# Kernel tuning notes

Measured on AMD Instinct MI355X. Metric: run time of the kernel, lower is better.

## Reference

```python
import jax, jax.numpy as jnp
import numpy as np
import math

A = 256            # n_agents == batch rows (epymarl stacks agents along batch)
B = A
OBS = 512          # obs_shape = (input_shape - n_actions) // 2
NA = 64            # n_actions
MSG = 2048         # messages_shape (divisible by A)
H = 1024           # hidden_dim
T = 3              # trajectory_length
TAU = OBS + NA
VD = MSG // A      # per-agent message dim


def setup_inputs() -> dict:
    key = jax.random.key(0)
    keys = iter(jax.random.split(key, 40))
    def lin(o, i):
        w = jax.random.normal(next(keys), (o, i), jnp.float32) * (i ** -0.5)
        return w, jnp.zeros((o,), jnp.float32)
    d = {}
    d["inputs"] = jax.random.normal(next(keys), (B, 2 * OBS + NA + MSG), jnp.float32)
    d["hidden_state"] = jax.random.normal(next(keys), (B, 3 * H), jnp.float32) * 0.1
    for name, o, i in [("pi_fc1", H, OBS + MSG), ("pi_fc2", NA, H),
                       ("fa_fc1", H, OBS), ("fa_fc2", (A - 1) * NA, H),
                       ("fo_fc1", H, NA * A + OBS), ("fo_fc2", OBS, H),
                       ("am_qs", H, MSG), ("am_ks", H, TAU), ("am_vs", VD, TAU)]:
        d[name + "_w"], d[name + "_b"] = lin(o, i)
    for name in ["pi_rnn", "fa_rnn", "fo_rnn"]:
        d[name + "_wih"], d[name + "_bih"] = lin(3 * H, H)
        d[name + "_whh"], d[name + "_bhh"] = lin(3 * H, H)
    return d


def _gru(x, h, wih, whh, bih, bhh):
    gi = x @ wih.T + bih
    gh = h @ whh.T + bhh
    ir, iz, i_n = jnp.split(gi, 3, -1)
    hr, hz, h_n = jnp.split(gh, 3, -1)
    r = jax.nn.sigmoid(ir + hr)
    z = jax.nn.sigmoid(iz + hz)
    n = jnp.tanh(i_n + r * h_n)
    return (1.0 - z) * n + z * h


def reference(inputs, hidden_state,
              pi_fc1_w, pi_fc1_b, pi_fc2_w, pi_fc2_b,
              pi_rnn_wih, pi_rnn_whh, pi_rnn_bih, pi_rnn_bhh,
              fa_fc1_w, fa_fc1_b, fa_fc2_w, fa_fc2_b,
              fa_rnn_wih, fa_rnn_whh, fa_rnn_bih, fa_rnn_bhh,
              fo_fc1_w, fo_fc1_b, fo_fc2_w, fo_fc2_b,
              fo_rnn_wih, fo_rnn_whh, fo_rnn_bih, fo_rnn_bhh,
              am_qs_w, am_qs_b, am_ks_w, am_ks_b, am_vs_w, am_vs_b):
    sg = jax.lax.stop_gradient
    lin = lambda x, w, b: x @ w.T + b
    h_fa = hidden_state[:, :H]
    h_fo = hidden_state[:, H:2 * H]
    h_pi0 = hidden_state[:, -H:]
    obs = inputs[:, :OBS]
    prev_obs = inputs[:, OBS:2 * OBS]
    prev_act = sg(inputs[:, 2 * OBS:2 * OBS + NA])   # .detach() in torch
    prev_msg = inputs[:, -MSG:]

    def pi(o, m, h):
        x = jax.nn.relu(lin(jnp.concatenate([o, m], -1), pi_fc1_w, pi_fc1_b))
        h2 = _gru(x, h, pi_rnn_wih, pi_rnn_whh, pi_rnn_bih, pi_rnn_bhh)
        return lin(h2, pi_fc2_w, pi_fc2_b), h2

    # ---- ImaginedTrajectory rollout (fixed small T, python loop is structural) ----
    o, a, h_pi = prev_obs, prev_act, h_pi0
    observations, actions = [o], [a]
    for _ in range(T - 1):
        x = jax.nn.relu(lin(o, fa_fc1_w, fa_fc1_b))
        h_fa = _gru(x, h_fa, fa_rnn_wih, fa_rnn_whh, fa_rnn_bih, fa_rnn_bhh)
        q = lin(h_fa, fa_fc2_w, fa_fc2_b)                       # [B,(A-1)*NA]
        qs = jax.nn.softmax(q.reshape(B, A - 1, NA), -1)
        # torch stack(qs_out).reshape(orig): scrambles (A-1,B) order, kept faithfully
        fa = jnp.transpose(qs, (1, 0, 2)).reshape(B, (A - 1) * NA)
        x2 = jax.nn.relu(lin(jnp.concatenate([fa, a, o], -1), fo_fc1_w, fo_fc1_b))
        h_fo = _gru(x2, h_fo, fo_rnn_wih, fo_rnn_whh, fo_rnn_bih, fo_rnn_bhh)
        nxt_o = lin(h_fo, fo_fc2_w, fo_fc2_b)
        nxt_a, h_pi = pi(sg(o), sg(prev_msg), sg(h_pi))         # forward_pi detaches inputs
        o, a = nxt_o, nxt_a
        observations.append(o)
        actions.append(a)
    taus = jnp.stack([jnp.concatenate([observations[t], actions[t]], -1)
                      for t in range(T)])                        # [T,B,TAU]

    # ---- AttentionMechanism: batched equivalent of the per-agent python loops ----
    # k rows are indexed j*n_agents + i with batch == n_agents, i.e. k[t, b] here.
    qv = lin(prev_msg, am_qs_w, am_qs_b)                         # [B,H]
    kk = jnp.einsum('tbi,hi->tbh', taus, am_ks_w) + am_ks_b      # [T,B,H]
    vv = jnp.einsum('tbi,vi->tbv', taus, am_vs_w) + am_vs_b      # [T,B,VD]
    alpha = jax.nn.softmax(jnp.einsum('bh,tbh->bt', qv, kk) / math.sqrt(H), -1)
    new_message = jnp.einsum('bt,tbv->bv', alpha, vv)            # [B,VD]

    # cat([msg]*A, 0).reshape(B,-1): each agent receives all agents' messages
    pi_msg = jnp.tile(new_message, (A, 1)).reshape(B, -1)        # [B,MSG]
    action, h_pi_f = pi(obs, pi_msg, h_pi0)                      # uses ORIGINAL h_pi slice
    h_out = jnp.concatenate([h_fa, h_fo, h_pi_f], -1)            # [B,3H]
    q_out = jnp.concatenate([new_message, action], -1)           # [B,VD+NA]
    return q_out, h_out
```

## Files before the change

kernel.cpp:

```cpp
#include <hip/hip_runtime.h>
#include <hip/hip_bf16.h>
#include <math.h>

#define OBS 512
#define MSG 2048
#define TAU 576
#define TAUP 640
#define QN 16320
#define X2W 16896
#define INW 3136
#define PIW 2560

typedef short short8v __attribute__((ext_vector_type(8)));
typedef float f32x4 __attribute__((ext_vector_type(4)));

__device__ inline unsigned bfbits(float x) {
  __hip_bfloat16 h = __float2bfloat16(x);
  return (unsigned)*reinterpret_cast<unsigned short*>(&h);
}

__device__ inline void gload16(const void* g, void* l) {
  __builtin_amdgcn_global_load_lds((__attribute__((address_space(1))) void*)(g),
                                   (__attribute__((address_space(3))) void*)(l), 16, 0, 0);
}

template<int ACT, bool ATOMIC>
__global__ __launch_bounds__(256)
void k_mfma(const __hip_bfloat16* __restrict__ A, int lda,
            const __hip_bfloat16* __restrict__ Wt, int ldw,
            const float* __restrict__ bias,
            float* __restrict__ C, int ldc,
            __hip_bfloat16* __restrict__ Cb, int ldcb,
            int Nlim, int nsteps)
{
  __shared__ __hip_bfloat16 As[2][64 * 128];
  __shared__ __hip_bfloat16 Bs[2][64 * 128];
  const int tid = threadIdx.x;
  const int lane = tid & 63;
  const int wid = tid >> 6;
  const int m0 = blockIdx.y * 64, n0 = blockIdx.x * 64;
  const int wr = wid >> 1, wc = wid & 1;
  const int fr = lane & 15, q = lane >> 4;
  const size_t k0 = (size_t)blockIdx.z * nsteps * 128;

  const __hip_bfloat16* Ab = A + (size_t)m0 * lda + k0;
  const __hip_bfloat16* Bb = Wt + (size_t)n0 * ldw + k0;

  int srow[4], scol[4], sdst[4];
#pragma unroll
  for (int r = 0; r < 4; ++r) {
    int chunk = r * 256 + tid;
    srow[r] = chunk >> 4;
    int c = chunk & 15;
    scol[r] = (c ^ (srow[r] & 7)) * 8;
    sdst[r] = chunk * 8;
  }

  const int arow0 = wr * 32 + fr, arow1 = arow0 + 16;
  const int brow0 = wc * 32 + fr, brow1 = brow0 + 16;
  const int amask = arow0 & 7, bmask = brow0 & 7;

  f32x4 acc[2][2] = {};

#pragma unroll
  for (int r = 0; r < 4; ++r)
    gload16(Ab + (size_t)srow[r] * lda + scol[r], &As[0][sdst[r]]);
#pragma unroll
  for (int r = 0; r < 4; ++r)
    gload16(Bb + (size_t)srow[r] * ldw + scol[r], &Bs[0][sdst[r]]);
  __syncthreads();

  for (int t = 0; t < nsteps; ++t) {
    if (t + 1 < nsteps) {
      const int kt = (t + 1) * 128;
      const int buf = (t + 1) & 1;
#pragma unroll
      for (int r = 0; r < 4; ++r)
        gload16(Ab + (size_t)srow[r] * lda + kt + scol[r], &As[buf][sdst[r]]);
#pragma unroll
      for (int r = 0; r < 4; ++r)
        gload16(Bb + (size_t)srow[r] * ldw + kt + scol[r], &Bs[buf][sdst[r]]);
    }
    const __hip_bfloat16* Ac = As[t & 1];
    const __hip_bfloat16* Bc = Bs[t & 1];
#pragma unroll
    for (int ks = 0; ks < 4; ++ks) {
      const int cc = ks * 4 + q;
      short8v a0 = *(const short8v*)&Ac[arow0 * 128 + ((cc ^ amask) << 3)];
      short8v a1 = *(const short8v*)&Ac[arow1 * 128 + ((cc ^ amask) << 3)];
      short8v b0 = *(const short8v*)&Bc[brow0 * 128 + ((cc ^ bmask) << 3)];
      short8v b1 = *(const short8v*)&Bc[brow1 * 128 + ((cc ^ bmask) << 3)];
      acc[0][0] = __builtin_amdgcn_mfma_f32_16x16x32_bf16(a0, b0, acc[0][0], 0, 0, 0);
      acc[0][1] = __builtin_amdgcn_mfma_f32_16x16x32_bf16(a0, b1, acc[0][1], 0, 0, 0);
      acc[1][0] = __builtin_amdgcn_mfma_f32_16x16x32_bf16(a1, b0, acc[1][0], 0, 0, 0);
      acc[1][1] = __builtin_amdgcn_mfma_f32_16x16x32_bf16(a1, b1, acc[1][1], 0, 0, 0);
    }
    __syncthreads();
  }

#pragma unroll
  for (int i = 0; i < 2; ++i) {
    const int mbase = m0 + wr * 32 + i * 16 + q * 4;
#pragma unroll
    for (int j = 0; j < 2; ++j) {
      const int n = n0 + wc * 32 + j * 16 + fr;
      if (n >= Nlim) continue;
      if (ATOMIC) {
#pragma unroll
        for (int v = 0; v < 4; ++v)
          atomicAdd(&C[(size_t)(mbase + v) * ldc + n], acc[i][j][v]);
      } else {
        const float bb = bias[n];
#pragma unroll
        for (int v = 0; v < 4; ++v) {
          float val = acc[i][j][v] + bb;
          if (ACT) val = fmaxf(val, 0.f);
          if (C)  C[(size_t)(mbase + v) * ldc + n] = val;
          if (Cb) Cb[(size_t)(mbase + v) * ldcb + n] = __float2bfloat16(val);
        }
      }
    }
  }
}

__global__ __launch_bounds__(256)
void k_cvtw(const float* __restrict__ src, int lds_, __hip_bfloat16* __restrict__ dst,
            int N, int Kdst, int Kval, int Npad)
{
  size_t idx = ((size_t)blockIdx.x * 256 + threadIdx.x) * 8;
  if (idx >= (size_t)Npad * Kdst) return;
  int n = (int)(idx / Kdst);
  int k = (int)(idx % Kdst);
  uint4 o;
  if (n < N && k < Kval) {
    const float* s = src + (size_t)n * lds_ + k;
    float4 v0 = *(const float4*)s;
    float4 v1 = *(const float4*)(s + 4);
    o.x = bfbits(v0.x) | (bfbits(v0.y) << 16);
    o.y = bfbits(v0.z) | (bfbits(v0.w) << 16);
    o.z = bfbits(v1.x) | (bfbits(v1.y) << 16);
    o.w = bfbits(v1.z) | (bfbits(v1.w) << 16);
  } else {
    o = make_uint4(0, 0, 0, 0);
  }
  *(uint4*)(dst + idx) = o;
}

__global__ __launch_bounds__(256)
void k_gru(const float* __restrict__ gi, const float* __restrict__ gh,
           const float* __restrict__ hs, int ldsrc,
           float* __restrict__ hd, int lddst, __hip_bfloat16* __restrict__ hb)
{
  int idx = blockIdx.x * 256 + threadIdx.x;
  int b = idx >> 10, j = idx & 1023;
  float ir = gi[b * 3072 + j];
  float iz = gi[b * 3072 + 1024 + j];
  float in_ = gi[b * 3072 + 2048 + j];
  float hr = gh[b * 3072 + j];
  float hz = gh[b * 3072 + 1024 + j];
  float hn = gh[b * 3072 + 2048 + j];
  float r = 1.f / (1.f + expf(-(ir + hr)));
  float z = 1.f / (1.f + expf(-(iz + hz)));
  float n = tanhf(in_ + r * hn);
  float h = hs[(size_t)b * ldsrc + j];
  float o = (1.f - z) * n + z * h;
  hd[(size_t)b * lddst + j] = o;
  hb[idx] = __float2bfloat16(o);
}

__global__ __launch_bounds__(256)
void k_softmax_scatter(const __hip_bfloat16* __restrict__ q, __hip_bfloat16* __restrict__ x2)
{
  int wid = blockIdx.x * 4 + (threadIdx.x >> 6);
  int lane = threadIdx.x & 63;
  int b = wid / 255, p = wid % 255;
  float v = __bfloat162float(q[(size_t)b * QN + p * 64 + lane]);
  float m = v;
#pragma unroll
  for (int s = 32; s; s >>= 1) m = fmaxf(m, __shfl_xor(m, s));
  float e = expf(v - m);
  float sum = e;
#pragma unroll
  for (int s = 32; s; s >>= 1) sum += __shfl_xor(sum, s);
  float r = e / sum;
  int flat = p * 16384 + b * 64 + lane;
  int bp = flat / QN;
  int j = flat - bp * QN;
  x2[(size_t)bp * X2W + j] = __float2bfloat16(r);
}

__global__ __launch_bounds__(256)
void k_x2_tail(const __hip_bfloat16* __restrict__ taus_t, __hip_bfloat16* __restrict__ x2)
{
  int idx = blockIdx.x * 256 + threadIdx.x;
  int b = idx / TAU, c = idx % TAU;
  if (c < 64)
    x2[(size_t)b * X2W + QN + c] = taus_t[(size_t)b * TAUP + OBS + c];
  else
    x2[(size_t)b * X2W + QN + 64 + (c - 64)] = taus_t[(size_t)b * TAUP + (c - 64)];
}

__global__ __launch_bounds__(256)
void k_concat_pi_loop(const __hip_bfloat16* __restrict__ taus_t,
                      const __hip_bfloat16* __restrict__ msg,
                      __hip_bfloat16* __restrict__ piin)
{
  int idx = blockIdx.x * 256 + threadIdx.x;
  int b = idx / PIW, c = idx % PIW;
  piin[idx] = (c < OBS) ? taus_t[(size_t)b * TAUP + c] : msg[b * MSG + (c - OBS)];
}

__global__ __launch_bounds__(256)
void k_concat_pi_final(const float* __restrict__ in, const float* __restrict__ nm,
                       __hip_bfloat16* __restrict__ piin)
{
  int idx = blockIdx.x * 256 + threadIdx.x;
  int b = idx / PIW, c = idx % PIW;
  float v = (c < OBS) ? in[(size_t)b * INW + c] : nm[c - OBS];
  piin[idx] = __float2bfloat16(v);
}

__global__ __launch_bounds__(256)
void k_init_h(const float* __restrict__ hid,
              float* __restrict__ h32a, float* __restrict__ h32o, float* __restrict__ h32p,
              __hip_bfloat16* __restrict__ hba, __hip_bfloat16* __restrict__ hbo,
              __hip_bfloat16* __restrict__ hbp, __hip_bfloat16* __restrict__ hbp0)
{
  int idx = blockIdx.x * 256 + threadIdx.x;
  int b = idx / 3072, c = idx % 3072;
  float v = hid[idx];
  __hip_bfloat16 hb = __float2bfloat16(v);
  int j = c & 1023;
  if (c < 1024)      { h32a[b * 1024 + j] = v; hba[b * 1024 + j] = hb; }
  else if (c < 2048) { h32o[b * 1024 + j] = v; hbo[b * 1024 + j] = hb; }
  else               { h32p[b * 1024 + j] = v; hbp[b * 1024 + j] = hb; hbp0[b * 1024 + j] = hb; }
}

__global__ __launch_bounds__(256)
void k_init_taus(const float* __restrict__ in, __hip_bfloat16* __restrict__ taus)
{
  int idx = blockIdx.x * 256 + threadIdx.x;
  int t = idx / (256 * TAUP);
  int r = (idx / TAUP) % 256;
  int c = idx % TAUP;
  float v = 0.f;
  if (t == 0 && c < TAU)
    v = (c < OBS) ? in[(size_t)r * INW + OBS + c]
                  : in[(size_t)r * INW + 2 * OBS + (c - OBS)];
  taus[idx] = __float2bfloat16(v);
}

__global__ __launch_bounds__(256)
void k_fill_bias(float* __restrict__ C, const float* __restrict__ bias)
{
  int idx = blockIdx.x * 256 + threadIdx.x;
  C[idx] = bias[idx & 1023];
}

__global__ __launch_bounds__(256)
void k_relu_cvt(const float* __restrict__ s, __hip_bfloat16* __restrict__ d)
{
  int idx = blockIdx.x * 256 + threadIdx.x;
  d[idx] = __float2bfloat16(fmaxf(s[idx], 0.f));
}

__global__ __launch_bounds__(64)
void k_vv(const __hip_bfloat16* __restrict__ taus, const float* __restrict__ w,
          const float* __restrict__ bias, float* __restrict__ vv)
{
  int row = blockIdx.x;
  int lane = threadIdx.x;
  const __hip_bfloat16* tr = taus + (size_t)row * TAUP;
  for (int v = 0; v < 8; ++v) {
    float s = 0.f;
    for (int k = lane; k < TAU; k += 64) s += __bfloat162float(tr[k]) * w[v * TAU + k];
#pragma unroll
    for (int d = 32; d; d >>= 1) s += __shfl_xor(s, d);
    if (lane == 0) vv[row * 8 + v] = s + bias[v];
  }
}

__global__ __launch_bounds__(64)
void k_attn(const float* __restrict__ qv, const float* __restrict__ kk,
            const float* __restrict__ vv, float* __restrict__ nm,
            float* __restrict__ out_q)
{
  int b = blockIdx.x;
  int lane = threadIdx.x;
  const float* qb = qv + (size_t)b * 1024;
  float s[3];
#pragma unroll
  for (int t = 0; t < 3; ++t) {
    const float* kb = kk + (size_t)(t * 256 + b) * 1024;
    float acc = 0.f;
    for (int h = lane; h < 1024; h += 64) acc += qb[h] * kb[h];
#pragma unroll
    for (int d = 32; d; d >>= 1) acc += __shfl_xor(acc, d);
    s[t] = acc * (1.f / 32.f);
  }
  float m = fmaxf(s[0], fmaxf(s[1], s[2]));
  float e0 = expf(s[0] - m), e1 = expf(s[1] - m), e2 = expf(s[2] - m);
  float inv = 1.f / (e0 + e1 + e2);
  float a0 = e0 * inv, a1 = e1 * inv, a2 = e2 * inv;
  if (lane < 8) {
    float v = a0 * vv[(0 * 256 + b) * 8 + lane]
            + a1 * vv[(1 * 256 + b) * 8 + lane]
            + a2 * vv[(2 * 256 + b) * 8 + lane];
    nm[b * 8 + lane] = v;
    out_q[b * 72 + lane] = v;
  }
}

__global__ __launch_bounds__(256)
void k_copy_hout(const float* __restrict__ hfa, const float* __restrict__ hfo,
                 float* __restrict__ hout)
{
  int idx = blockIdx.x * 256 + threadIdx.x;
  int b = idx / 2048, c = idx % 2048;
  float v = (c < 1024) ? hfa[b * 1024 + c] : hfo[b * 1024 + (c - 1024)];
  hout[(size_t)b * 3072 + c] = v;
}

extern "C" void kernel_launch(void* const* d_in, const int* in_sizes, int n_in,
                              void* d_out_v, int out_size, void* d_ws, size_t ws_size,
                              hipStream_t stream)
{
  const float* inputs   = (const float*)d_in[0];
  const float* hidden   = (const float*)d_in[1];
  const float* pi_fc1_w = (const float*)d_in[2];
  const float* pi_fc1_b = (const float*)d_in[3];
  const float* pi_fc2_w = (const float*)d_in[4];
  const float* pi_fc2_b = (const float*)d_in[5];
  const float* fa_fc1_w = (const float*)d_in[6];
  const float* fa_fc1_b = (const float*)d_in[7];
  const float* fa_fc2_w = (const float*)d_in[8];
  const float* fa_fc2_b = (const float*)d_in[9];
  const float* fo_fc1_w = (const float*)d_in[10];
  const float* fo_fc1_b = (const float*)d_in[11];
  const float* fo_fc2_w = (const float*)d_in[12];
  const float* fo_fc2_b = (const float*)d_in[13];
  const float* am_qs_w  = (const float*)d_in[14];
  const float* am_qs_b  = (const float*)d_in[15];
  const float* am_ks_w  = (const float*)d_in[16];
  const float* am_ks_b  = (const float*)d_in[17];
  const float* am_vs_w  = (const float*)d_in[18];
  const float* am_vs_b  = (const float*)d_in[19];
  const float* pi_wih   = (const float*)d_in[20];
  const float* pi_bih   = (const float*)d_in[21];
  const float* pi_whh   = (const float*)d_in[22];
  const float* pi_bhh   = (const float*)d_in[23];
  const float* fa_wih   = (const float*)d_in[24];
  const float* fa_bih   = (const float*)d_in[25];
  const float* fa_whh   = (const float*)d_in[26];
  const float* fa_bhh   = (const float*)d_in[27];
  const float* fo_wih   = (const float*)d_in[28];
  const float* fo_bih   = (const float*)d_in[29];
  const float* fo_whh   = (const float*)d_in[30];
  const float* fo_bhh   = (const float*)d_in[31];

  float* out = (float*)d_out_v;
  char* p = (char*)d_ws;
  auto alloc = [&](size_t bytes) { void* r = p; p += (bytes + 255) & ~(size_t)255; return r; };
  typedef __hip_bfloat16 bf;

  bf* WPI1 = (bf*)alloc((size_t)1024 * 2560 * 2);
  bf* WPI2 = (bf*)alloc((size_t)64 * 1024 * 2);
  bf* WFA1 = (bf*)alloc((size_t)1024 * 512 * 2);
  bf* WFA2 = (bf*)alloc((size_t)16320 * 1024 * 2);
  bf* WFO1 = (bf*)alloc((size_t)1024 * 16896 * 2);
  bf* WFO2 = (bf*)alloc((size_t)512 * 1024 * 2);
  bf* WQS  = (bf*)alloc((size_t)1024 * 2048 * 2);
  bf* WKS  = (bf*)alloc((size_t)1024 * TAUP * 2);
  bf* WPIIH = (bf*)alloc((size_t)3072 * 1024 * 2);
  bf* WPIHH = (bf*)alloc((size_t)3072 * 1024 * 2);
  bf* WFAIH = (bf*)alloc((size_t)3072 * 1024 * 2);
  bf* WFAHH = (bf*)alloc((size_t)3072 * 1024 * 2);
  bf* WFOIH = (bf*)alloc((size_t)3072 * 1024 * 2);
  bf* WFOHH = (bf*)alloc((size_t)3072 * 1024 * 2);
  bf* HFAB = (bf*)alloc((size_t)256 * 1024 * 2);
  bf* HFOB = (bf*)alloc((size_t)256 * 1024 * 2);
  bf* HPIB = (bf*)alloc((size_t)256 * 1024 * 2);
  bf* HPI0B = (bf*)alloc((size_t)256 * 1024 * 2);
  bf* XBUFB = (bf*)alloc((size_t)256 * 1024 * 2);
  bf* TAUSB = (bf*)alloc((size_t)3 * 256 * TAUP * 2);
  bf* X2B  = (bf*)alloc((size_t)256 * X2W * 2);
  bf* PIINB = (bf*)alloc((size_t)256 * PIW * 2);
  bf* MSGB = (bf*)alloc((size_t)256 * MSG * 2);
  bf* QBUFB = (bf*)alloc((size_t)256 * QN * 2);
  float* HFA32 = (float*)alloc((size_t)256 * 1024 * 4);
  float* HFO32 = (float*)alloc((size_t)256 * 1024 * 4);
  float* HPI32 = (float*)alloc((size_t)256 * 1024 * 4);
  float* XBUF32 = (float*)alloc((size_t)256 * 1024 * 4);
  float* GI = (float*)alloc((size_t)256 * 3072 * 4);
  float* GH = (float*)alloc((size_t)256 * 3072 * 4);
  float* QV = (float*)alloc((size_t)256 * 1024 * 4);
  float* KK = (float*)alloc((size_t)768 * 1024 * 4);
  float* VV = (float*)alloc((size_t)768 * 8 * 4);
  float* NM = (float*)alloc((size_t)2048 * 4);

  auto cvt = [&](const float* src, int srcld, bf* dst, int N, int Kdst, int Kval, int Npad) {
    size_t total = ((size_t)Npad * Kdst) / 8;
    int blocks = (int)((total + 255) / 256);
    k_cvtw<<<blocks, 256, 0, stream>>>(src, srcld, dst, N, Kdst, Kval, Npad);
  };
  auto mm = [&](const bf* Aa, int lda, const bf* Ww, int ldw, const float* bias,
                float* C, int ldc, bf* Cb, int ldcb,
                int M, int Npad, int Nlim, int K, int act) {
    dim3 g(Npad / 64, M / 64, 1);
    int nsteps = K / 128;
    if (act) k_mfma<1, false><<<g, 256, 0, stream>>>(Aa, lda, Ww, ldw, bias, C, ldc, Cb, ldcb, Nlim, nsteps);
    else     k_mfma<0, false><<<g, 256, 0, stream>>>(Aa, lda, Ww, ldw, bias, C, ldc, Cb, ldcb, Nlim, nsteps);
  };

  cvt(pi_fc1_w, 2560, WPI1, 1024, 2560, 2560, 1024);
  cvt(pi_fc2_w, 1024, WPI2, 64, 1024, 1024, 64);
  cvt(fa_fc1_w, 512,  WFA1, 1024, 512, 512, 1024);
  cvt(fa_fc2_w, 1024, WFA2, 16320, 1024, 1024, 16320);
  cvt(fo_fc1_w, 16896, WFO1, 1024, 16896, 16896, 1024);
  cvt(fo_fc2_w, 1024, WFO2, 512, 1024, 1024, 512);
  cvt(am_qs_w, 2048, WQS, 1024, 2048, 2048, 1024);
  cvt(am_ks_w, 576, WKS, 1024, TAUP, 576, 1024);
  cvt(pi_wih, 1024, WPIIH, 3072, 1024, 1024, 3072);
  cvt(pi_whh, 1024, WPIHH, 3072, 1024, 1024, 3072);
  cvt(fa_wih, 1024, WFAIH, 3072, 1024, 1024, 3072);
  cvt(fa_whh, 1024, WFAHH, 3072, 1024, 1024, 3072);
  cvt(fo_wih, 1024, WFOIH, 3072, 1024, 1024, 3072);
  cvt(fo_whh, 1024, WFOHH, 3072, 1024, 1024, 3072);
  cvt(inputs + 1088, INW, MSGB, 256, 2048, 2048, 256);

  k_init_h<<<3072, 256, 0, stream>>>(hidden, HFA32, HFO32, HPI32, HFAB, HFOB, HPIB, HPI0B);
  k_init_taus<<<3 * TAUP, 256, 0, stream>>>(inputs, TAUSB);

  for (int t = 0; t < 2; ++t) {
    bf* taus_t = TAUSB + (size_t)t * 256 * TAUP;
    bf* taus_n = TAUSB + (size_t)(t + 1) * 256 * TAUP;
    mm(taus_t, TAUP, WFA1, 512, fa_fc1_b, nullptr, 0, XBUFB, 1024, 256, 1024, 1024, 512, 1);
    mm(XBUFB, 1024, WFAIH, 1024, fa_bih, GI, 3072, nullptr, 0, 256, 3072, 3072, 1024, 0);
    mm(HFAB, 1024, WFAHH, 1024, fa_bhh, GH, 3072, nullptr, 0, 256, 3072, 3072, 1024, 0);
    k_gru<<<1024, 256, 0, stream>>>(GI, GH, HFA32, 1024, HFA32, 1024, HFAB);
    mm(HFAB, 1024, WFA2, 1024, fa_fc2_b, nullptr, 0, QBUFB, QN, 256, QN, QN, 1024, 0);
    k_x2_tail<<<576, 256, 0, stream>>>(taus_t, X2B);
    k_softmax_scatter<<<16320, 256, 0, stream>>>(QBUFB, X2B);
    k_fill_bias<<<1024, 256, 0, stream>>>(XBUF32, fo_fc1_b);
    {
      dim3 g(1024 / 64, 256 / 64, 12);
      k_mfma<0, true><<<g, 256, 0, stream>>>(X2B, X2W, WFO1, X2W, nullptr,
                                             XBUF32, 1024, nullptr, 0, 1024, 11);
    }
    k_relu_cvt<<<1024, 256, 0, stream>>>(XBUF32, XBUFB);
    mm(XBUFB, 1024, WFOIH, 1024, fo_bih, GI, 3072, nullptr, 0, 256, 3072, 3072, 1024, 0);
    mm(HFOB, 1024, WFOHH, 1024, fo_bhh, GH, 3072, nullptr, 0, 256, 3072, 3072, 1024, 0);
    k_gru<<<1024, 256, 0, stream>>>(GI, GH, HFO32, 1024, HFO32, 1024, HFOB);
    mm(HFOB, 1024, WFO2, 1024, fo_fc2_b, nullptr, 0, taus_n, TAUP, 256, 512, 512, 1024, 0);
    k_concat_pi_loop<<<2560, 256, 0, stream>>>(taus_t, MSGB, PIINB);
    mm(PIINB, PIW, WPI1, PIW, pi_fc1_b, nullptr, 0, XBUFB, 1024, 256, 1024, 1024, 2560, 1);
    mm(XBUFB, 1024, WPIIH, 1024, pi_bih, GI, 3072, nullptr, 0, 256, 3072, 3072, 1024, 0);
    mm(HPIB, 1024, WPIHH, 1024, pi_bhh, GH, 3072, nullptr, 0, 256, 3072, 3072, 1024, 0);
    k_gru<<<1024, 256, 0, stream>>>(GI, GH, HPI32, 1024, HPI32, 1024, HPIB);
    mm(HPIB, 1024, WPI2, 1024, pi_fc2_b, nullptr, 0, taus_n + OBS, TAUP, 256, 64, 64, 1024, 0);
  }

  mm(MSGB, MSG, WQS, MSG, am_qs_b, QV, 1024, nullptr, 0, 256, 1024, 1024, 2048, 0);
  mm(TAUSB, TAUP, WKS, TAUP, am_ks_b, KK, 1024, nullptr, 0, 768, 1024, 1024, TAUP, 0);
  k_vv<<<768, 64, 0, stream>>>(TAUSB, am_vs_w, am_vs_b, VV);
  k_attn<<<256, 64, 0, stream>>>(QV, KK, VV, NM, out);

  k_concat_pi_final<<<2560, 256, 0, stream>>>(inputs, NM, PIINB);
  mm(PIINB, PIW, WPI1, PIW, pi_fc1_b, nullptr, 0, XBUFB, 1024, 256, 1024, 1024, 2560, 1);
  mm(XBUFB, 1024, WPIIH, 1024, pi_bih, GI, 3072, nullptr, 0, 256, 3072, 3072, 1024, 0);
  mm(HPI0B, 1024, WPIHH, 1024, pi_bhh, GH, 3072, nullptr, 0, 256, 3072, 3072, 1024, 0);
  k_gru<<<1024, 256, 0, stream>>>(GI, GH, hidden + 2048, 3072,
                                  out + 256 * 72 + 2048, 3072, HPIB);
  mm(HPIB, 1024, WPI2, 1024, pi_fc2_b, out + 8, 72, nullptr, 0, 256, 64, 64, 1024, 0);
  k_copy_hout<<<2048, 256, 0, stream>>>(HFA32, HFO32, out + 256 * 72);
  (void)in_sizes; (void)n_in; (void)out_size; (void)ws_size;
}
```

Before: 626.2 us.

## Retile GEMM to 256x64 blocks, fuse GRU gate GEMMs, batch weight conversion

```diff
diff --git a/kernel.cpp b/kernel.cpp
--- a/kernel.cpp
+++ b/kernel.cpp
@@ -24,83 +24,89 @@
                                    (__attribute__((address_space(3))) void*)(l), 16, 0, 0);
 }
 
-template<int ACT, bool ATOMIC>
-__global__ __launch_bounds__(256)
-void k_mfma(const __hip_bfloat16* __restrict__ A, int lda,
-            const __hip_bfloat16* __restrict__ Wt, int ldw,
-            const float* __restrict__ bias,
-            float* __restrict__ C, int ldc,
-            __hip_bfloat16* __restrict__ Cb, int ldcb,
-            int Nlim, int nsteps)
-{
-  __shared__ __hip_bfloat16 As[2][64 * 128];
-  __shared__ __hip_bfloat16 Bs[2][64 * 128];
+struct MMSet {
+  const __hip_bfloat16* A;
+  const __hip_bfloat16* W;
+  const float* bias;
+  float* C;
+  __hip_bfloat16* Cb;
+  int lda, ldw, ldc, ldcb;
+};
+
+template<int ACT, bool ATOMIC, bool DUAL>
+__global__ __launch_bounds__(512)
+void k_mm(MMSet s0, MMSet s1, int Nlim, int kSteps)
+{
+  __shared__ __hip_bfloat16 As[2][256 * 64];
+  __shared__ __hip_bfloat16 Bs[2][64 * 64];
+  const MMSet S = (DUAL && blockIdx.z) ? s1 : s0;
   const int tid = threadIdx.x;
   const int lane = tid & 63;
   const int wid = tid >> 6;
-  const int m0 = blockIdx.y * 64, n0 = blockIdx.x * 64;
+  const int m0 = blockIdx.y * 256;
+  const int n0 = blockIdx.x * 64;
+  const size_t k0 = ATOMIC ? (size_t)blockIdx.z * kSteps * 64 : 0;
+
+  const __hip_bfloat16* Ab = S.A + (size_t)m0 * S.lda + k0;
+  const __hip_bfloat16* Bb = S.W + (size_t)n0 * S.ldw + k0;
+
+  int arow[4], acol[4], adst[4];
+#pragma unroll
+  for (int r = 0; r < 4; ++r) {
+    int chunk = r * 512 + tid;
+    arow[r] = chunk >> 3;
+    acol[r] = ((chunk & 7) ^ (arow[r] & 7)) * 8;
+    adst[r] = chunk * 8;
+  }
+  const int brow = tid >> 3;
+  const int bcol = ((tid & 7) ^ (brow & 7)) * 8;
+  const int bdst = tid * 8;
+
   const int wr = wid >> 1, wc = wid & 1;
   const int fr = lane & 15, q = lane >> 4;
-  const size_t k0 = (size_t)blockIdx.z * nsteps * 128;
-
-  const __hip_bfloat16* Ab = A + (size_t)m0 * lda + k0;
-  const __hip_bfloat16* Bb = Wt + (size_t)n0 * ldw + k0;
-
-  int srow[4], scol[4], sdst[4];
-#pragma unroll
-  for (int r = 0; r < 4; ++r) {
-    int chunk = r * 256 + tid;
-    srow[r] = chunk >> 4;
-    int c = chunk & 15;
-    scol[r] = (c ^ (srow[r] & 7)) * 8;
-    sdst[r] = chunk * 8;
-  }
-
-  const int arow0 = wr * 32 + fr, arow1 = arow0 + 16;
-  const int brow0 = wc * 32 + fr, brow1 = brow0 + 16;
-  const int amask = arow0 & 7, bmask = brow0 & 7;
-
-  f32x4 acc[2][2] = {};
-
-#pragma unroll
-  for (int r = 0; r < 4; ++r)
-    gload16(Ab + (size_t)srow[r] * lda + scol[r], &As[0][sdst[r]]);
-#pragma unroll
-  for (int r = 0; r < 4; ++r)
-    gload16(Bb + (size_t)srow[r] * ldw + scol[r], &Bs[0][sdst[r]]);
+  const int xm = fr & 7;
+
+  f32x4 acc[4][2] = {};
+
+  auto stage = [&](int buf, int kt) {
+#pragma unroll
+    for (int r = 0; r < 4; ++r)
+      gload16(Ab + (size_t)arow[r] * S.lda + kt + acol[r], &As[buf][adst[r]]);
+    gload16(Bb + (size_t)brow * S.ldw + kt + bcol, &Bs[buf][bdst]);
+  };
+
+  stage(0, 0);
   __syncthreads();
 
-  for (int t = 0; t < nsteps; ++t) {
-    if (t + 1 < nsteps) {
-      const int kt = (t + 1) * 128;
-      const int buf = (t + 1) & 1;
-#pragma unroll
-      for (int r = 0; r < 4; ++r)
-        gload16(Ab + (size_t)srow[r] * lda + kt + scol[r], &As[buf][sdst[r]]);
-#pragma unroll
-      for (int r = 0; r < 4; ++r)
-        gload16(Bb + (size_t)srow[r] * ldw + kt + scol[r], &Bs[buf][sdst[r]]);
-    }
+  for (int t = 0; t < kSteps; ++t) {
+    if (t + 1 < kSteps) stage((t + 1) & 1, (t + 1) * 64);
     const __hip_bfloat16* Ac = As[t & 1];
     const __hip_bfloat16* Bc = Bs[t & 1];
 #pragma unroll
-    for (int ks = 0; ks < 4; ++ks) {
+    for (int ks = 0; ks < 2; ++ks) {
       const int cc = ks * 4 + q;
-      short8v a0 = *(const short8v*)&Ac[arow0 * 128 + ((cc ^ amask) << 3)];
-      short8v a1 = *(const short8v*)&Ac[arow1 * 128 + ((cc ^ amask) << 3)];
-      short8v b0 = *(const short8v*)&Bc[brow0 * 128 + ((cc ^ bmask) << 3)];
-      short8v b1 = *(const short8v*)&Bc[brow1 * 128 + ((cc ^ bmask) << 3)];
+      const int co = ((cc ^ xm) << 3);
+      short8v a0 = *(const short8v*)&Ac[(wr * 64 +  0 + fr) * 64 + co];
+      short8v a1 = *(const short8v*)&Ac[(wr * 64 + 16 + fr) * 64 + co];
+      short8v a2 = *(const short8v*)&Ac[(wr * 64 + 32 + fr) * 64 + co];
+      short8v a3 = *(const short8v*)&Ac[(wr * 64 + 48 + fr) * 64 + co];
+      short8v b0 = *(const short8v*)&Bc[(wc * 32 +  0 + fr) * 64 + co];
+      short8v b1 = *(const short8v*)&Bc[(wc * 32 + 16 + fr) * 64 + co];
       acc[0][0] = __builtin_amdgcn_mfma_f32_16x16x32_bf16(a0, b0, acc[0][0], 0, 0, 0);
       acc[0][1] = __builtin_amdgcn_mfma_f32_16x16x32_bf16(a0, b1, acc[0][1], 0, 0, 0);
       acc[1][0] = __builtin_amdgcn_mfma_f32_16x16x32_bf16(a1, b0, acc[1][0], 0, 0, 0);
       acc[1][1] = __builtin_amdgcn_mfma_f32_16x16x32_bf16(a1, b1, acc[1][1], 0, 0, 0);
+      acc[2][0] = __builtin_amdgcn_mfma_f32_16x16x32_bf16(a2, b0, acc[2][0], 0, 0, 0);
+      acc[2][1] = __builtin_amdgcn_mfma_f32_16x16x32_bf16(a2, b1, acc[2][1], 0, 0, 0);
+      acc[3][0] = __builtin_amdgcn_mfma_f32_16x16x32_bf16(a3, b0, acc[3][0], 0, 0, 0);
+      acc[3][1] = __builtin_amdgcn_mfma_f32_16x16x32_bf16(a3, b1, acc[3][1], 0, 0, 0);
     }
     __syncthreads();
   }
 
 #pragma unroll
-  for (int i = 0; i < 2; ++i) {
-    const int mbase = m0 + wr * 32 + i * 16 + q * 4;
+  for (int i = 0; i < 4; ++i) {
+    const int mb = m0 + wr * 64 + i * 16 + q * 4;
 #pragma unroll
     for (int j = 0; j < 2; ++j) {
       const int n = n0 + wc * 32 + j * 16 + fr;
@@ -108,32 +114,51 @@
       if (ATOMIC) {
 #pragma unroll
         for (int v = 0; v < 4; ++v)
-          atomicAdd(&C[(size_t)(mbase + v) * ldc + n], acc[i][j][v]);
+          atomicAdd(&S.C[(size_t)(mb + v) * S.ldc + n], acc[i][j][v]);
       } else {
-        const float bb = bias[n];
+        const float bb = S.bias[n];
 #pragma unroll
         for (int v = 0; v < 4; ++v) {
           float val = acc[i][j][v] + bb;
           if (ACT) val = fmaxf(val, 0.f);
-          if (C)  C[(size_t)(mbase + v) * ldc + n] = val;
-          if (Cb) Cb[(size_t)(mbase + v) * ldcb + n] = __float2bfloat16(val);
+          if (S.C)  S.C[(size_t)(mb + v) * S.ldc + n] = val;
+          if (S.Cb) S.Cb[(size_t)(mb + v) * S.ldcb + n] = __float2bfloat16(val);
         }
       }
     }
   }
 }
 
-__global__ __launch_bounds__(256)
-void k_cvtw(const float* __restrict__ src, int lds_, __hip_bfloat16* __restrict__ dst,
-            int N, int Kdst, int Kval, int Npad)
-{
-  size_t idx = ((size_t)blockIdx.x * 256 + threadIdx.x) * 8;
-  if (idx >= (size_t)Npad * Kdst) return;
-  int n = (int)(idx / Kdst);
-  int k = (int)(idx % Kdst);
+struct CvtTable {
+  const float* src[15];
+  __hip_bfloat16* dst[15];
+  long nchunk[15];
+  int srcld[15], N[15], Kdst[15], Kval[15];
+  int cumBlk[16];
+};
+
+__global__ __launch_bounds__(256)
+void k_cvt_all(CvtTable T)
+{
+  const int bx = blockIdx.x;
+  int sg = 0;
+#pragma unroll
+  for (int i = 1; i < 15; ++i) sg += (bx >= T.cumBlk[i]) ? 1 : 0;
+  const float* src = T.src[0]; __hip_bfloat16* dst = T.dst[0];
+  long nchunk = T.nchunk[0];
+  int srcld = T.srcld[0], N = T.N[0], Kd = T.Kdst[0], Kv = T.Kval[0], b0 = T.cumBlk[0];
+#pragma unroll
+  for (int i = 1; i < 15; ++i)
+    if (sg == i) { src = T.src[i]; dst = T.dst[i]; nchunk = T.nchunk[i];
+                   srcld = T.srcld[i]; N = T.N[i]; Kd = T.Kdst[i]; Kv = T.Kval[i]; b0 = T.cumBlk[i]; }
+  long chunk = (long)(bx - b0) * 256 + threadIdx.x;
+  if (chunk >= nchunk) return;
+  long idx = chunk * 8;
+  int n = (int)(idx / Kd);
+  int k = (int)(idx % Kd);
   uint4 o;
-  if (n < N && k < Kval) {
-    const float* s = src + (size_t)n * lds_ + k;
+  if (n < N && k < Kv) {
+    const float* s = src + (size_t)n * srcld + k;
     float4 v0 = *(const float4*)s;
     float4 v1 = *(const float4*)(s + 4);
     o.x = bfbits(v0.x) | (bfbits(v0.y) << 16);
@@ -366,7 +391,7 @@
   bf* WPI1 = (bf*)alloc((size_t)1024 * 2560 * 2);
   bf* WPI2 = (bf*)alloc((size_t)64 * 1024 * 2);
   bf* WFA1 = (bf*)alloc((size_t)1024 * 512 * 2);
-  bf* WFA2 = (bf*)alloc((size_t)16320 * 1024 * 2);
+  bf* WFA2 = (bf*)alloc((size_t)16384 * 1024 * 2);
   bf* WFO1 = (bf*)alloc((size_t)1024 * 16896 * 2);
   bf* WFO2 = (bf*)alloc((size_t)512 * 1024 * 2);
   bf* WQS  = (bf*)alloc((size_t)1024 * 2048 * 2);
@@ -398,80 +423,93 @@
   float* VV = (float*)alloc((size_t)768 * 8 * 4);
   float* NM = (float*)alloc((size_t)2048 * 4);
 
-  auto cvt = [&](const float* src, int srcld, bf* dst, int N, int Kdst, int Kval, int Npad) {
-    size_t total = ((size_t)Npad * Kdst) / 8;
-    int blocks = (int)((total + 255) / 256);
-    k_cvtw<<<blocks, 256, 0, stream>>>(src, srcld, dst, N, Kdst, Kval, Npad);
+  CvtTable T;
+  int nseg = 0; int blk = 0;
+  auto addseg = [&](const float* src, int srcld, bf* dst, int N, int Kdst, int Kval, int Npad) {
+    long ch = (long)Npad * Kdst / 8;
+    T.src[nseg] = src; T.dst[nseg] = dst; T.nchunk[nseg] = ch;
+    T.srcld[nseg] = srcld; T.N[nseg] = N; T.Kdst[nseg] = Kdst; T.Kval[nseg] = Kval;
+    T.cumBlk[nseg] = blk;
+    blk += (int)((ch + 255) / 256);
+    ++nseg;
   };
-  auto mm = [&](const bf* Aa, int lda, const bf* Ww, int ldw, const float* bias,
-                float* C, int ldc, bf* Cb, int ldcb,
-                int M, int Npad, int Nlim, int K, int act) {
-    dim3 g(Npad / 64, M / 64, 1);
-    int nsteps = K / 128;
-    if (act) k_mfma<1, false><<<g, 256, 0, stream>>>(Aa, lda, Ww, ldw, bias, C, ldc, Cb, ldcb, Nlim, nsteps);
-    else     k_mfma<0, false><<<g, 256, 0, stream>>>(Aa, lda, Ww, ldw, bias, C, ldc, Cb, ldcb, Nlim, nsteps);
+  addseg(pi_fc1_w, 2560, WPI1, 1024, 2560, 2560, 1024);
+  addseg(pi_fc2_w, 1024, WPI2, 64, 1024, 1024, 64);
+  addseg(fa_fc1_w, 512,  WFA1, 1024, 512, 512, 1024);
+  addseg(fa_fc2_w, 1024, WFA2, 16320, 1024, 1024, 16384);
+  addseg(fo_fc1_w, 16896, WFO1, 1024, 16896, 16896, 1024);
+  addseg(fo_fc2_w, 1024, WFO2, 512, 1024, 1024, 512);
+  addseg(am_qs_w, 2048, WQS, 1024, 2048, 2048, 1024);
+  addseg(am_ks_w, 576, WKS, 1024, TAUP, 576, 1024);
+  addseg(pi_wih, 1024, WPIIH, 3072, 1024, 1024, 3072);
+  addseg(pi_whh, 1024, WPIHH, 3072, 1024, 1024, 3072);
+  addseg(fa_wih, 1024, WFAIH, 3072, 1024, 1024, 3072);
+  addseg(fa_whh, 1024, WFAHH, 3072, 1024, 1024, 3072);
+  addseg(fo_wih, 1024, WFOIH, 3072, 1024, 1024, 3072);
+  addseg(fo_whh, 1024, WFOHH, 3072, 1024, 1024, 3072);
+  addseg(inputs + 1088, INW, MSGB, 256, 2048, 2048, 256);
+  T.cumBlk[15] = blk;
+
+  auto mset = [&](const bf* A, int lda, const bf* W, int ldw, const float* bias,
+                  float* C, int ldc, bf* Cb, int ldcb) {
+    MMSet s; s.A = A; s.W = W; s.bias = bias; s.C = C; s.Cb = Cb;
+    s.lda = lda; s.ldw = ldw; s.ldc = ldc; s.ldcb = ldcb; return s;
   };
-
-  cvt(pi_fc1_w, 2560, WPI1, 1024, 2560, 2560, 1024);
-  cvt(pi_fc2_w, 1024, WPI2, 64, 1024, 1024, 64);
-  cvt(fa_fc1_w, 512,  WFA1, 1024, 512, 512, 1024);
-  cvt(fa_fc2_w, 1024, WFA2, 16320, 1024, 1024, 16320);
-  cvt(fo_fc1_w, 16896, WFO1, 1024, 16896, 16896, 1024);
-  cvt(fo_fc2_w, 1024, WFO2, 512, 1024, 1024, 512);
-  cvt(am_qs_w, 2048, WQS, 1024, 2048, 2048, 1024);
-  cvt(am_ks_w, 576, WKS, 1024, TAUP, 576, 1024);
-  cvt(pi_wih, 1024, WPIIH, 3072, 1024, 1024, 3072);
-  cvt(pi_whh, 1024, WPIHH, 3072, 1024, 1024, 3072);
-  cvt(fa_wih, 1024, WFAIH, 3072, 1024, 1024, 3072);
-  cvt(fa_whh, 1024, WFAHH, 3072, 1024, 1024, 3072);
-  cvt(fo_wih, 1024, WFOIH, 3072, 1024, 1024, 3072);
-  cvt(fo_whh, 1024, WFOHH, 3072, 1024, 1024, 3072);
-  cvt(inputs + 1088, INW, MSGB, 256, 2048, 2048, 256);
-
+  auto mm = [&](MMSet a, int M, int Npad, int Nlim, int K, int act) {
+    dim3 g(Npad / 64, M / 256, 1);
+    if (act) k_mm<1, false, false><<<g, 512, 0, stream>>>(a, a, Nlim, K / 64);
+    else     k_mm<0, false, false><<<g, 512, 0, stream>>>(a, a, Nlim, K / 64);
+  };
+  auto mmDual = [&](MMSet a, MMSet b, int Npad, int K) {
+    dim3 g(Npad / 64, 1, 2);
+    k_mm<0, false, true><<<g, 512, 0, stream>>>(a, b, Npad, K / 64);
+  };
+
+  k_cvt_all<<<blk, 256, 0, stream>>>(T);
   k_init_h<<<3072, 256, 0, stream>>>(hidden, HFA32, HFO32, HPI32, HFAB, HFOB, HPIB, HPI0B);
   k_init_taus<<<3 * TAUP, 256, 0, stream>>>(inputs, TAUSB);
 
   for (int t = 0; t < 2; ++t) {
     bf* taus_t = TAUSB + (size_t)t * 256 * TAUP;
     bf* taus_n = TAUSB + (size_t)(t + 1) * 256 * TAUP;
-    mm(taus_t, TAUP, WFA1, 512, fa_fc1_b, nullptr, 0, XBUFB, 1024, 256, 1024, 1024, 512, 1);
-    mm(XBUFB, 1024, WFAIH, 1024, fa_bih, GI, 3072, nullptr, 0, 256, 3072, 3072, 1024, 0);
-    mm(HFAB, 1024, WFAHH, 1024, fa_bhh, GH, 3072, nullptr, 0, 256, 3072, 3072, 1024, 0);
+    mm(mset(taus_t, TAUP, WFA1, 512, fa_fc1_b, nullptr, 0, XBUFB, 1024), 256, 1024, 1024, 512, 1);
+    mmDual(mset(XBUFB, 1024, WFAIH, 1024, fa_bih, GI, 3072, nullptr, 0),
+           mset(HFAB, 1024, WFAHH, 1024, fa_bhh, GH, 3072, nullptr, 0), 3072, 1024);
     k_gru<<<1024, 256, 0, stream>>>(GI, GH, HFA32, 1024, HFA32, 1024, HFAB);
-    mm(HFAB, 1024, WFA2, 1024, fa_fc2_b, nullptr, 0, QBUFB, QN, 256, QN, QN, 1024, 0);
+    mm(mset(HFAB, 1024, WFA2, 1024, fa_fc2_b, nullptr, 0, QBUFB, QN), 256, 16384, QN, 1024, 0);
     k_x2_tail<<<576, 256, 0, stream>>>(taus_t, X2B);
     k_softmax_scatter<<<16320, 256, 0, stream>>>(QBUFB, X2B);
     k_fill_bias<<<1024, 256, 0, stream>>>(XBUF32, fo_fc1_b);
     {
-      dim3 g(1024 / 64, 256 / 64, 12);
-      k_mfma<0, true><<<g, 256, 0, stream>>>(X2B, X2W, WFO1, X2W, nullptr,
-                                             XBUF32, 1024, nullptr, 0, 1024, 11);
+      dim3 g(16, 1, 12);
+      MMSet s = mset(X2B, X2W, WFO1, X2W, fo_fc1_b, XBUF32, 1024, nullptr, 0);
+      k_mm<0, true, false><<<g, 512, 0, stream>>>(s, s, 1024, 22);
     }
     k_relu_cvt<<<1024, 256, 0, stream>>>(XBUF32, XBUFB);
-    mm(XBUFB, 1024, WFOIH, 1024, fo_bih, GI, 3072, nullptr, 0, 256, 3072, 3072, 1024, 0);
-    mm(HFOB, 1024, WFOHH, 1024, fo_bhh, GH, 3072, nullptr, 0, 256, 3072, 3072, 1024, 0);
+    mmDual(mset(XBUFB, 1024, WFOIH, 1024, fo_bih, GI, 3072, nullptr, 0),
+           mset(HFOB, 1024, WFOHH, 1024, fo_bhh, GH, 3072, nullptr, 0), 3072, 1024);
     k_gru<<<1024, 256, 0, stream>>>(GI, GH, HFO32, 1024, HFO32, 1024, HFOB);
-    mm(HFOB, 1024, WFO2, 1024, fo_fc2_b, nullptr, 0, taus_n, TAUP, 256, 512, 512, 1024, 0);
+    mm(mset(HFOB, 1024, WFO2, 1024, fo_fc2_b, nullptr, 0, taus_n, TAUP), 256, 512, 512, 1024, 0);
     k_concat_pi_loop<<<2560, 256, 0, stream>>>(taus_t, MSGB, PIINB);
-    mm(PIINB, PIW, WPI1, PIW, pi_fc1_b, nullptr, 0, XBUFB, 1024, 256, 1024, 1024, 2560, 1);
-    mm(XBUFB, 1024, WPIIH, 1024, pi_bih, GI, 3072, nullptr, 0, 256, 3072, 3072, 1024, 0);
-    mm(HPIB, 1024, WPIHH, 1024, pi_bhh, GH, 3072, nullptr, 0, 256, 3072, 3072, 1024, 0);
+    mm(mset(PIINB, PIW, WPI1, PIW, pi_fc1_b, nullptr, 0, XBUFB, 1024), 256, 1024, 1024, PIW, 1);
+    mmDual(mset(XBUFB, 1024, WPIIH, 1024, pi_bih, GI, 3072, nullptr, 0),
+           mset(HPIB, 1024, WPIHH, 1024, pi_bhh, GH, 3072, nullptr, 0), 3072, 1024);
     k_gru<<<1024, 256, 0, stream>>>(GI, GH, HPI32, 1024, HPI32, 1024, HPIB);
-    mm(HPIB, 1024, WPI2, 1024, pi_fc2_b, nullptr, 0, taus_n + OBS, TAUP, 256, 64, 64, 1024, 0);
-  }
-
-  mm(MSGB, MSG, WQS, MSG, am_qs_b, QV, 1024, nullptr, 0, 256, 1024, 1024, 2048, 0);
-  mm(TAUSB, TAUP, WKS, TAUP, am_ks_b, KK, 1024, nullptr, 0, 768, 1024, 1024, TAUP, 0);
+    mm(mset(HPIB, 1024, WPI2, 1024, pi_fc2_b, nullptr, 0, taus_n + OBS, TAUP), 256, 64, 64, 1024, 0);
+  }
+
+  mm(mset(MSGB, MSG, WQS, MSG, am_qs_b, QV, 1024, nullptr, 0), 256, 1024, 1024, 2048, 0);
+  mm(mset(TAUSB, TAUP, WKS, TAUP, am_ks_b, KK, 1024, nullptr, 0), 768, 1024, 1024, TAUP, 0);
   k_vv<<<768, 64, 0, stream>>>(TAUSB, am_vs_w, am_vs_b, VV);
   k_attn<<<256, 64, 0, stream>>>(QV, KK, VV, NM, out);
 
   k_concat_pi_final<<<2560, 256, 0, stream>>>(inputs, NM, PIINB);
-  mm(PIINB, PIW, WPI1, PIW, pi_fc1_b, nullptr, 0, XBUFB, 1024, 256, 1024, 1024, 2560, 1);
-  mm(XBUFB, 1024, WPIIH, 1024, pi_bih, GI, 3072, nullptr, 0, 256, 3072, 3072, 1024, 0);
-  mm(HPI0B, 1024, WPIHH, 1024, pi_bhh, GH, 3072, nullptr, 0, 256, 3072, 3072, 1024, 0);
+  mm(mset(PIINB, PIW, WPI1, PIW, pi_fc1_b, nullptr, 0, XBUFB, 1024), 256, 1024, 1024, PIW, 1);
+  mmDual(mset(XBUFB, 1024, WPIIH, 1024, pi_bih, GI, 3072, nullptr, 0),
+         mset(HPI0B, 1024, WPIHH, 1024, pi_bhh, GH, 3072, nullptr, 0), 3072, 1024);
   k_gru<<<1024, 256, 0, stream>>>(GI, GH, hidden + 2048, 3072,
                                   out + 256 * 72 + 2048, 3072, HPIB);
-  mm(HPIB, 1024, WPI2, 1024, pi_fc2_b, out + 8, 72, nullptr, 0, 256, 64, 64, 1024, 0);
+  mm(mset(HPIB, 1024, WPI2, 1024, pi_fc2_b, out + 8, 72, nullptr, 0), 256, 64, 64, 1024, 0);
   k_copy_hout<<<2048, 256, 0, stream>>>(HFA32, HFO32, out + 256 * 72);
   (void)in_sizes; (void)n_in; (void)out_size; (void)ws_size;
 }
```

Measured after the change: 736.8 us. +17.7%, slower.
